# Optimization experiments

Measured on AMD Instinct MI355X. Metric: run time of the kernel, lower is better.

## Reference

```python
import jax, jax.numpy as jnp
import numpy as np

NUM_EMBEDDINGS = 1024
EMBEDDING_DIM = 64
COMMITMENT_COST = 0.25
DECAY = 0.99
EPS = 1e-5


def setup_inputs() -> dict:
    key = jax.random.key(0)
    k1, k2 = jax.random.split(key)
    inputs = jax.random.normal(k1, (32, EMBEDDING_DIM, 64, 64), dtype=jnp.float32)
    scale = 1.0 / NUM_EMBEDDINGS
    embeddings = jax.random.uniform(k2, (NUM_EMBEDDINGS, EMBEDDING_DIM),
                                    dtype=jnp.float32, minval=-scale, maxval=scale)
    return {
        "inputs": inputs,
        "embeddings": embeddings,
        "ema_cluster_size": jnp.zeros((NUM_EMBEDDINGS,), dtype=jnp.float32),
        "ema_w": embeddings.copy(),
    }


def reference(inputs, embeddings, ema_cluster_size, ema_w):
    sg = jax.lax.stop_gradient
    B, C, H, W = inputs.shape          # C == embedding_dim
    K, D = embeddings.shape

    # [B,C,H,W] -> [N,D]
    flat = jnp.transpose(inputs, (0, 2, 3, 1)).reshape(-1, D)

    distances = (jnp.sum(flat * flat, axis=1, keepdims=True)
                 + jnp.sum(embeddings * embeddings, axis=1)
                 - 2.0 * flat @ embeddings.T)
    encoding_indices = jnp.argmin(distances, axis=1)  # [N]

    quantized = embeddings[encoding_indices].reshape(B, H, W, C)
    quantized = jnp.transpose(quantized, (0, 3, 1, 2))  # [B,C,H,W]

    e_latent_loss = jnp.mean((sg(quantized) - inputs) ** 2)
    q_latent_loss = jnp.mean((quantized - sg(inputs)) ** 2)
    vq_loss = q_latent_loss + COMMITMENT_COST * e_latent_loss

    # --- EMA codebook update (no-grad side effect in original) ---
    flat_ng = sg(flat)
    counts = jax.ops.segment_sum(jnp.ones_like(encoding_indices, dtype=flat.dtype),
                                 encoding_indices, num_segments=K)  # == one_hot.sum(0)
    new_cluster_size = ema_cluster_size * DECAY + (1.0 - DECAY) * counts
    # scatter-add of inputs per code (replaces wasteful N*K*D one-hot broadcast)
    embedded_sum = jax.ops.segment_sum(flat_ng, encoding_indices, num_segments=K)
    new_ema_w = ema_w * DECAY + (1.0 - DECAY) * embedded_sum
    n = jnp.sum(new_cluster_size)
    cluster_size = (new_cluster_size + EPS) / (n + K * EPS) * n
    new_embeddings = new_ema_w / cluster_size[:, None]

    # straight-through estimator
    quantized_st = inputs + sg(quantized - inputs)

    return (quantized_st, vq_loss, encoding_indices.reshape(B, H, W),
            new_cluster_size, new_ema_w, new_embeddings)
```

## Files before the change

### kernel.cpp

```cpp
#include <hip/hip_runtime.h>

#define NUM_K 1024
#define DIM 64
#define HWSZ 4096
#define NPIX 131072

#define OUT_Q    0u
#define OUT_LOSS 8388608u
#define OUT_IDX  8388609u
#define OUT_CS   8519681u
#define OUT_EMAW 8520705u
#define OUT_EMB  8586241u

#define WS_SE    0
#define WS_CNT   1024
#define WS_ESUM  2048
#define WS_LOSS  67584
#define WS_NSUM  67585
#define WS_EBF   67840
#define WS_ZERO_BEG 1024
#define WS_ZERO_LEN 66562

#define PIXB   128
#define MARGIN 1.6e-3f

using bf16x8 = __attribute__((ext_vector_type(8))) short;
using f32x4  = __attribute__((ext_vector_type(4))) float;

__device__ __forceinline__ unsigned short f2bf(float f) {
    unsigned u = __float_as_uint(f);
    u += 0x7FFFu + ((u >> 16) & 1u);
    return (unsigned short)(u >> 16);
}

__device__ __forceinline__ float np_sumsq64(const float* __restrict__ a) {
#pragma clang fp contract(off)
    float r0 = a[0] * a[0], r1 = a[1] * a[1], r2 = a[2] * a[2], r3 = a[3] * a[3];
    float r4 = a[4] * a[4], r5 = a[5] * a[5], r6 = a[6] * a[6], r7 = a[7] * a[7];
    for (int i = 8; i < 64; i += 8) {
        r0 += a[i + 0] * a[i + 0];
        r1 += a[i + 1] * a[i + 1];
        r2 += a[i + 2] * a[i + 2];
        r3 += a[i + 3] * a[i + 3];
        r4 += a[i + 4] * a[i + 4];
        r5 += a[i + 5] * a[i + 5];
        r6 += a[i + 6] * a[i + 6];
        r7 += a[i + 7] * a[i + 7];
    }
    return ((r0 + r1) + (r2 + r3)) + ((r4 + r5) + (r6 + r7));
}

__device__ __forceinline__ float np_sumsq64_s(const float* __restrict__ a, int stride) {
#pragma clang fp contract(off)
    float r[8];
#pragma unroll
    for (int j = 0; j < 8; ++j) { const float v = a[j * stride]; r[j] = v * v; }
#pragma unroll
    for (int i = 8; i < 64; i += 8)
#pragma unroll
        for (int j = 0; j < 8; ++j) { const float v = a[(i + j) * stride]; r[j] += v * v; }
    return ((r[0] + r[1]) + (r[2] + r[3])) + ((r[4] + r[5]) + (r[6] + r[7]));
}

__global__ __launch_bounds__(256) void vq_init(const float* __restrict__ emb,
                                               float* __restrict__ ws) {
    const int t = blockIdx.x * 256 + threadIdx.x;
    if (t < WS_ZERO_LEN) ws[WS_ZERO_BEG + t] = 0.0f;
    if (t < NUM_K) ws[WS_SE + t] = np_sumsq64(emb + t * DIM);
    if (t < 8192) {
        const int ct = t >> 7, h = (t >> 6) & 1, ln = t & 63;
        const int code = ct * 16 + (ln & 15), g = ln >> 4;
        const float* er = emb + code * DIM + h * 32 + g * 8;
        unsigned s[8];
#pragma unroll
        for (int e = 0; e < 8; ++e) s[e] = f2bf(er[e]);
        uint4 v = make_uint4(s[0] | (s[1] << 16), s[2] | (s[3] << 16),
                             s[4] | (s[5] << 16), s[6] | (s[7] << 16));
        ((uint4*)(ws + WS_EBF))[t] = v;
    }
}

__global__ __launch_bounds__(256) void vq_main(const float* __restrict__ in,
                                               const float* __restrict__ emb,
                                               float* __restrict__ out,
                                               float* __restrict__ ws) {
    __shared__ __align__(16) float xF[DIM * 132];
    __shared__ __align__(16) float SeL[NUM_K];
    __shared__ float          redM[4][PIXB];
    __shared__ int            cnt_l[PIXB];
    __shared__ unsigned short cand[PIXB * 12];
    __shared__ int            bk[PIXB];
    __shared__ float          wred[4];

    const int t    = threadIdx.x;
    const int lane = t & 63, w = t >> 6;
    const int g    = lane >> 4, cpix = lane & 15;
    const int bid  = blockIdx.x;
    const int b    = bid >> 5;
    const int hw0  = (bid & 31) << 7;
    const int n0   = bid << 7;

    const float* inb = in + (size_t)b * (DIM * HWSZ);

    {
        const float4* s4 = (const float4*)(inb + hw0);
#pragma unroll
        for (int i = 0; i < 8; ++i) {
            const int fi = t + i * 256;
            const int d = fi >> 5, p4 = fi & 31;
            *(float4*)&xF[d * 132 + p4 * 4] = s4[(size_t)d * 1024 + p4];
        }
        ((float4*)SeL)[t] = ((const float4*)(ws + WS_SE))[t];
        if (t < PIXB) cnt_l[t] = 0;
    }
    __syncthreads();

    bf16x8 Bfr[8][2];
#pragma unroll
    for (int tt = 0; tt < 8; ++tt) {
        const int p = tt * 16 + cpix;
#pragma unroll
        for (int h = 0; h < 2; ++h) {
            bf16x8 v;
#pragma unroll
            for (int e = 0; e < 8; ++e)
                v[e] = (short)f2bf(xF[(h * 32 + g * 8 + e) * 132 + p]);
            Bfr[tt][h] = v;
        }
    }
    float Sx = 0.0f;
    if (t < PIXB) Sx = np_sumsq64_s(xF + t, 132);

    const bf16x8* Ef  = (const bf16x8*)(ws + WS_EBF);
    const int     ct0 = w << 4;

    float mn[8];
#pragma unroll
    for (int tt = 0; tt < 8; ++tt) mn[tt] = 3.4e38f;

#pragma unroll 4
    for (int ci = 0; ci < 16; ++ci) {
        const int ct = ct0 + ci;
        const bf16x8 A0 = Ef[(ct * 2 + 0) * 64 + lane];
        const bf16x8 A1 = Ef[(ct * 2 + 1) * 64 + lane];
        const f32x4  se = *(const f32x4*)&SeL[(ct << 4) + (g << 2)];
#pragma unroll
        for (int tt = 0; tt < 8; ++tt) {
            f32x4 acc = {0.f, 0.f, 0.f, 0.f};
            acc = __builtin_amdgcn_mfma_f32_16x16x32_bf16(A0, Bfr[tt][0], acc, 0, 0, 0);
            acc = __builtin_amdgcn_mfma_f32_16x16x32_bf16(A1, Bfr[tt][1], acc, 0, 0, 0);
            const float s0 = fmaf(-2.0f, acc[0], se[0]);
            const float s1 = fmaf(-2.0f, acc[1], se[1]);
            const float s2 = fmaf(-2.0f, acc[2], se[2]);
            const float s3 = fmaf(-2.0f, acc[3], se[3]);
            mn[tt] = fminf(mn[tt], fminf(fminf(s0, s1), fminf(s2, s3)));
        }
    }

#pragma unroll
    for (int tt = 0; tt < 8; ++tt) {
        float m2 = mn[tt];
        m2 = fminf(m2, __shfl_xor(m2, 16, 64));
        m2 = fminf(m2, __shfl_xor(m2, 32, 64));
        if (g == 0) redM[w][tt * 16 + cpix] = m2;
    }
    __syncthreads();
    float thr[8];
#pragma unroll
    for (int tt = 0; tt < 8; ++tt) {
        const int p = tt * 16 + cpix;
        thr[tt] = fminf(fminf(redM[0][p], redM[1][p]),
                        fminf(redM[2][p], redM[3][p])) + MARGIN;
    }

#pragma unroll 4
    for (int ci = 0; ci < 16; ++ci) {
        const int ct = ct0 + ci;
        const bf16x8 A0 = Ef[(ct * 2 + 0) * 64 + lane];
        const bf16x8 A1 = Ef[(ct * 2 + 1) * 64 + lane];
        const f32x4  se = *(const f32x4*)&SeL[(ct << 4) + (g << 2)];
#pragma unroll
        for (int tt = 0; tt < 8; ++tt) {
            f32x4 acc = {0.f, 0.f, 0.f, 0.f};
            acc = __builtin_amdgcn_mfma_f32_16x16x32_bf16(A0, Bfr[tt][0], acc, 0, 0, 0);
            acc = __builtin_amdgcn_mfma_f32_16x16x32_bf16(A1, Bfr[tt][1], acc, 0, 0, 0);
#pragma unroll
            for (int r = 0; r < 4; ++r) {
                const float s = fmaf(-2.0f, acc[r], se[r]);
                if (s <= thr[tt]) {
                    const int p    = tt * 16 + cpix;
                    const int code = (ct << 4) + (g << 2) + r;
                    const int sl   = atomicAdd(&cnt_l[p], 1);
                    if (sl < 12) cand[p * 12 + sl] = (unsigned short)code;
                }
            }
        }
    }
    __syncthreads();

    if (t < PIXB) {
        const int c  = t;
        const int cc = min(cnt_l[c], 12);
        float bd = 3.4e38f; int bi = NUM_K;
        for (int j = 0; j < cc; ++j) {
            const int cd = cand[c * 12 + j];
            const float4* er = (const float4*)(emb + cd * DIM);
            float dot = 0.0f;
#pragma unroll
            for (int i = 0; i < 16; ++i) {
                const float4 e4 = er[i];
                dot = fmaf(xF[(4 * i + 0) * 132 + c], e4.x, dot);
                dot = fmaf(xF[(4 * i + 1) * 132 + c], e4.y, dot);
                dot = fmaf(xF[(4 * i + 2) * 132 + c], e4.z, dot);
                dot = fmaf(xF[(4 * i + 3) * 132 + c], e4.w, dot);
            }
            const float Sec = SeL[cd];
            float dk;
            {
#pragma clang fp contract(off)
                const float tt2 = Sx + Sec;
                dk = tt2 - 2.0f * dot;
            }
            if (dk < bd || (dk == bd && cd < bi)) { bd = dk; bi = cd; }
        }
        bk[c] = bi;
        out[OUT_IDX + n0 + c] = (float)bi;
        atomicAdd(ws + WS_CNT + bi, 1.0f);
    }
    __syncthreads();

    float lsum = 0.0f;
    {
        const int px = t & 127, dh = t >> 7;
        const int id = bk[px];
        float* qp = out + OUT_Q + (size_t)b * (DIM * HWSZ) + hw0 + px;
        const float4* eb4 = (const float4*)(emb + (id << 6) + (dh << 5));
#pragma unroll
        for (int i = 0; i < 8; ++i) {
            const float4 e4 = eb4[i];
            const float ev[4] = {e4.x, e4.y, e4.z, e4.w};
#pragma unroll
            for (int q = 0; q < 4; ++q) {
                const int d = (dh << 5) + i * 4 + q;
                qp[(size_t)d * HWSZ] = ev[q];
                const float df = ev[q] - xF[d * 132 + px];
                lsum = fmaf(df, df, lsum);
            }
        }
    }
#pragma unroll
    for (int off = 32; off > 0; off >>= 1) lsum += __shfl_down(lsum, off, 64);
    if (lane == 0) wred[w] = lsum;
    __syncthreads();
    if (t == 0) atomicAdd(ws + WS_LOSS, (wred[0] + wred[1]) + (wred[2] + wred[3]));

    {
        float* es = ws + WS_ESUM;
#pragma unroll 1
        for (int j = 0; j < 32; ++j) {
            const int p   = (w << 5) + j;
            const int pid = bk[p];
            atomicAdd(es + (pid << 6) + lane, xF[lane * 132 + p]);
        }
    }
}

__global__ __launch_bounds__(256) void vq_cs(const float* __restrict__ ema_cs,
                                             float* __restrict__ out,
                                             float* __restrict__ ws) {
    const int k = blockIdx.x * 256 + threadIdx.x;
    const float ncs = fmaf(0.01f, ws[WS_CNT + k], 0.99f * ema_cs[k]);
    out[OUT_CS + k] = ncs;
    float s = ncs;
#pragma unroll
    for (int off = 32; off > 0; off >>= 1) s += __shfl_down(s, off, 64);
    if ((threadIdx.x & 63) == 0) atomicAdd(ws + WS_NSUM, s);
}

__global__ __launch_bounds__(256) void vq_final_b(const float* __restrict__ ema_w,
                                                  float* __restrict__ out,
                                                  float* __restrict__ ws) {
    const int i = blockIdx.x * 256 + threadIdx.x;
    const int k = i >> 6;
    const float nsum = ws[WS_NSUM];
    const float ncs  = out[OUT_CS + k];
    const float csz  = (ncs + 1e-5f) / (nsum + 1024.0f * 1e-5f) * nsum;
    const float nw   = fmaf(0.01f, ws[WS_ESUM + i], 0.99f * ema_w[i]);
    out[OUT_EMAW + i] = nw;
    out[OUT_EMB  + i] = nw / csz;
    if (i == 0) out[OUT_LOSS] = 1.25f * ws[WS_LOSS] * (1.0f / 8388608.0f);
}

extern "C" void kernel_launch(void* const* d_in, const int* in_sizes, int n_in,
                              void* d_out, int out_size, void* d_ws, size_t ws_size,
                              hipStream_t stream) {
    const float* in   = (const float*)d_in[0];
    const float* emb  = (const float*)d_in[1];
    const float* ecs  = (const float*)d_in[2];
    const float* emaw = (const float*)d_in[3];
    float* out = (float*)d_out;
    float* ws  = (float*)d_ws;

    vq_init<<<261, 256, 0, stream>>>(emb, ws);
    vq_main<<<NPIX / PIXB, 256, 0, stream>>>(in, emb, out, ws);
    vq_cs<<<4, 256, 0, stream>>>(ecs, out, ws);
    vq_final_b<<<256, 256, 0, stream>>>(emaw, out, ws);
}
```

Before: 216.0 us.

## Halve pixels per block, pad smem stride, fuse cluster-size kernel into final

Cuts the per-block pixel tile from 128 to 64, which doubles the grid to 2048 blocks and halves per-thread B fragments and LDS use. It sets launch bounds to request 5 waves-per-EU-level occupancy and changes the xF stride to 65 to avoid bank conflicts. It also folds the cluster-size kernel into the final kernel: each block redundantly recomputes the total count sum, which removes one launch and one global atomic. In exchange, every codebook fragment is reloaded from global for only half as many pixels, and the scalar LDS stores replace float4 stores.

```diff
diff --git a/kernel.cpp b/kernel.cpp
--- a/kernel.cpp
+++ b/kernel.cpp
@@ -16,12 +16,12 @@
 #define WS_CNT   1024
 #define WS_ESUM  2048
 #define WS_LOSS  67584
-#define WS_NSUM  67585
 #define WS_EBF   67840
 #define WS_ZERO_BEG 1024
-#define WS_ZERO_LEN 66562
-
-#define PIXB   128
+#define WS_ZERO_LEN 66561
+
+#define PIXB   64
+#define XSTR   65
 #define MARGIN 1.6e-3f
 
 using bf16x8 = __attribute__((ext_vector_type(8))) short;
@@ -80,13 +80,13 @@
     }
 }
 
-__global__ __launch_bounds__(256) void vq_main(const float* __restrict__ in,
-                                               const float* __restrict__ emb,
-                                               float* __restrict__ out,
-                                               float* __restrict__ ws) {
-    __shared__ __align__(16) float xF[DIM * 132];
-    __shared__ __align__(16) float SeL[NUM_K];
-    __shared__ float          redM[4][PIXB];
+__global__ __launch_bounds__(256, 5) void vq_main(const float* __restrict__ in,
+                                                  const float* __restrict__ emb,
+                                                  float* __restrict__ out,
+                                                  float* __restrict__ ws) {
+    __shared__ float xF[DIM * XSTR];
+    __shared__ float SeL[NUM_K];
+    __shared__ float redM[4][PIXB];
     __shared__ int            cnt_l[PIXB];
     __shared__ unsigned short cand[PIXB * 12];
     __shared__ int            bk[PIXB];
@@ -96,47 +96,49 @@
     const int lane = t & 63, w = t >> 6;
     const int g    = lane >> 4, cpix = lane & 15;
     const int bid  = blockIdx.x;
-    const int b    = bid >> 5;
-    const int hw0  = (bid & 31) << 7;
-    const int n0   = bid << 7;
+    const int b    = bid >> 6;
+    const int hw0  = (bid & 63) << 6;
+    const int n0   = bid << 6;
 
     const float* inb = in + (size_t)b * (DIM * HWSZ);
 
     {
         const float4* s4 = (const float4*)(inb + hw0);
 #pragma unroll
-        for (int i = 0; i < 8; ++i) {
+        for (int i = 0; i < 4; ++i) {
             const int fi = t + i * 256;
-            const int d = fi >> 5, p4 = fi & 31;
-            *(float4*)&xF[d * 132 + p4 * 4] = s4[(size_t)d * 1024 + p4];
+            const int d = fi >> 4, p4 = fi & 15;
+            const float4 v = s4[(size_t)d * 1024 + p4];
+            float* dst = &xF[d * XSTR + p4 * 4];
+            dst[0] = v.x; dst[1] = v.y; dst[2] = v.z; dst[3] = v.w;
         }
         ((float4*)SeL)[t] = ((const float4*)(ws + WS_SE))[t];
         if (t < PIXB) cnt_l[t] = 0;
     }
     __syncthreads();
 
-    bf16x8 Bfr[8][2];
-#pragma unroll
-    for (int tt = 0; tt < 8; ++tt) {
+    bf16x8 Bfr[4][2];
+#pragma unroll
+    for (int tt = 0; tt < 4; ++tt) {
         const int p = tt * 16 + cpix;
 #pragma unroll
         for (int h = 0; h < 2; ++h) {
             bf16x8 v;
 #pragma unroll
             for (int e = 0; e < 8; ++e)
-                v[e] = (short)f2bf(xF[(h * 32 + g * 8 + e) * 132 + p]);
+                v[e] = (short)f2bf(xF[(h * 32 + g * 8 + e) * XSTR + p]);
             Bfr[tt][h] = v;
         }
     }
     float Sx = 0.0f;
-    if (t < PIXB) Sx = np_sumsq64_s(xF + t, 132);
+    if (t < PIXB) Sx = np_sumsq64_s(xF + t, XSTR);
 
     const bf16x8* Ef  = (const bf16x8*)(ws + WS_EBF);
     const int     ct0 = w << 4;
 
-    float mn[8];
-#pragma unroll
-    for (int tt = 0; tt < 8; ++tt) mn[tt] = 3.4e38f;
+    float mn[4];
+#pragma unroll
+    for (int tt = 0; tt < 4; ++tt) mn[tt] = 3.4e38f;
 
 #pragma unroll 4
     for (int ci = 0; ci < 16; ++ci) {
@@ -145,7 +147,7 @@
         const bf16x8 A1 = Ef[(ct * 2 + 1) * 64 + lane];
         const f32x4  se = *(const f32x4*)&SeL[(ct << 4) + (g << 2)];
 #pragma unroll
-        for (int tt = 0; tt < 8; ++tt) {
+        for (int tt = 0; tt < 4; ++tt) {
             f32x4 acc = {0.f, 0.f, 0.f, 0.f};
             acc = __builtin_amdgcn_mfma_f32_16x16x32_bf16(A0, Bfr[tt][0], acc, 0, 0, 0);
             acc = __builtin_amdgcn_mfma_f32_16x16x32_bf16(A1, Bfr[tt][1], acc, 0, 0, 0);
@@ -153,21 +155,21 @@
             const float s1 = fmaf(-2.0f, acc[1], se[1]);
             const float s2 = fmaf(-2.0f, acc[2], se[2]);
             const float s3 = fmaf(-2.0f, acc[3], se[3]);
-            mn[tt] = fminf(mn[tt], fminf(fminf(s0, s1), fminf(s2, s3)));
-        }
-    }
-
-#pragma unroll
-    for (int tt = 0; tt < 8; ++tt) {
+            mn[tt] = fminf(fminf(fminf(s0, s1), fminf(s2, s3)), mn[tt]);
+        }
+    }
+
+#pragma unroll
+    for (int tt = 0; tt < 4; ++tt) {
         float m2 = mn[tt];
         m2 = fminf(m2, __shfl_xor(m2, 16, 64));
         m2 = fminf(m2, __shfl_xor(m2, 32, 64));
         if (g == 0) redM[w][tt * 16 + cpix] = m2;
     }
     __syncthreads();
-    float thr[8];
-#pragma unroll
-    for (int tt = 0; tt < 8; ++tt) {
+    float thr[4];
+#pragma unroll
+    for (int tt = 0; tt < 4; ++tt) {
         const int p = tt * 16 + cpix;
         thr[tt] = fminf(fminf(redM[0][p], redM[1][p]),
                         fminf(redM[2][p], redM[3][p])) + MARGIN;
@@ -178,12 +180,12 @@
         const int ct = ct0 + ci;
         const bf16x8 A0 = Ef[(ct * 2 + 0) * 64 + lane];
         const bf16x8 A1 = Ef[(ct * 2 + 1) * 64 + lane];
-        const f32x4  se = *(const f32x4*)&SeL[(ct << 4) + (g << 2)];
-#pragma unroll
-        for (int tt = 0; tt < 8; ++tt) {
+#pragma unroll
+        for (int tt = 0; tt < 4; ++tt) {
             f32x4 acc = {0.f, 0.f, 0.f, 0.f};
             acc = __builtin_amdgcn_mfma_f32_16x16x32_bf16(A0, Bfr[tt][0], acc, 0, 0, 0);
             acc = __builtin_amdgcn_mfma_f32_16x16x32_bf16(A1, Bfr[tt][1], acc, 0, 0, 0);
+            const f32x4 se = *(const f32x4*)&SeL[(ct << 4) + (g << 2)];
 #pragma unroll
             for (int r = 0; r < 4; ++r) {
                 const float s = fmaf(-2.0f, acc[r], se[r]);
@@ -209,10 +211,10 @@
 #pragma unroll
             for (int i = 0; i < 16; ++i) {
                 const float4 e4 = er[i];
-                dot = fmaf(xF[(4 * i + 0) * 132 + c], e4.x, dot);
-                dot = fmaf(xF[(4 * i + 1) * 132 + c], e4.y, dot);
-                dot = fmaf(xF[(4 * i + 2) * 132 + c], e4.z, dot);
-                dot = fmaf(xF[(4 * i + 3) * 132 + c], e4.w, dot);
+                dot = fmaf(xF[(4 * i + 0) * XSTR + c], e4.x, dot);
+                dot = fmaf(xF[(4 * i + 1) * XSTR + c], e4.y, dot);
+                dot = fmaf(xF[(4 * i + 2) * XSTR + c], e4.z, dot);
+                dot = fmaf(xF[(4 * i + 3) * XSTR + c], e4.w, dot);
             }
             const float Sec = SeL[cd];
             float dk;
@@ -231,19 +233,19 @@
 
     float lsum = 0.0f;
     {
-        const int px = t & 127, dh = t >> 7;
+        const int px = t & 63, dq = t >> 6;
         const int id = bk[px];
         float* qp = out + OUT_Q + (size_t)b * (DIM * HWSZ) + hw0 + px;
-        const float4* eb4 = (const float4*)(emb + (id << 6) + (dh << 5));
-#pragma unroll
-        for (int i = 0; i < 8; ++i) {
+        const float4* eb4 = (const float4*)(emb + (id << 6) + (dq << 4));
+#pragma unroll
+        for (int i = 0; i < 4; ++i) {
             const float4 e4 = eb4[i];
             const float ev[4] = {e4.x, e4.y, e4.z, e4.w};
 #pragma unroll
             for (int q = 0; q < 4; ++q) {
-                const int d = (dh << 5) + i * 4 + q;
+                const int d = (dq << 4) + i * 4 + q;
                 qp[(size_t)d * HWSZ] = ev[q];
-                const float df = ev[q] - xF[d * 132 + px];
+                const float df = ev[q] - xF[d * XSTR + px];
                 lsum = fmaf(df, df, lsum);
             }
         }
@@ -257,35 +259,46 @@
     {
         float* es = ws + WS_ESUM;
 #pragma unroll 1
-        for (int j = 0; j < 32; ++j) {
-            const int p   = (w << 5) + j;
+        for (int j = 0; j < 16; ++j) {
+            const int p   = (w << 4) + j;
             const int pid = bk[p];
-            atomicAdd(es + (pid << 6) + lane, xF[lane * 132 + p]);
-        }
-    }
-}
-
-__global__ __launch_bounds__(256) void vq_cs(const float* __restrict__ ema_cs,
-                                             float* __restrict__ out,
-                                             float* __restrict__ ws) {
-    const int k = blockIdx.x * 256 + threadIdx.x;
+            atomicAdd(es + (pid << 6) + lane, xF[lane * XSTR + p]);
+        }
+    }
+}
+
+__global__ __launch_bounds__(256) void vq_final(const float* __restrict__ ema_cs,
+                                                const float* __restrict__ ema_w,
+                                                float* __restrict__ out,
+                                                float* __restrict__ ws) {
+    __shared__ float nred[4];
+    const int t = threadIdx.x, lane = t & 63, w = t >> 6;
+
+    float s = 0.0f;
+#pragma unroll
+    for (int j = 0; j < 4; ++j) {
+        const int k = t + j * 256;
+        s += fmaf(0.01f, ws[WS_CNT + k], 0.99f * ema_cs[k]);
+    }
+#pragma unroll
+    for (int off = 32; off > 0; off >>= 1) s += __shfl_down(s, off, 64);
+    if (lane == 0) nred[w] = s;
+    __syncthreads();
+    const float nsum = (nred[0] + nred[1]) + (nred[2] + nred[3]);
+
+    if (blockIdx.x == 0) {
+#pragma unroll
+        for (int j = 0; j < 4; ++j) {
+            const int k = t + j * 256;
+            out[OUT_CS + k] = fmaf(0.01f, ws[WS_CNT + k], 0.99f * ema_cs[k]);
+        }
+    }
+
+    const int i = blockIdx.x * 256 + t;
+    const int k = i >> 6;
     const float ncs = fmaf(0.01f, ws[WS_CNT + k], 0.99f * ema_cs[k]);
-    out[OUT_CS + k] = ncs;
-    float s = ncs;
-#pragma unroll
-    for (int off = 32; off > 0; off >>= 1) s += __shfl_down(s, off, 64);
-    if ((threadIdx.x & 63) == 0) atomicAdd(ws + WS_NSUM, s);
-}
-
-__global__ __launch_bounds__(256) void vq_final_b(const float* __restrict__ ema_w,
-                                                  float* __restrict__ out,
-                                                  float* __restrict__ ws) {
-    const int i = blockIdx.x * 256 + threadIdx.x;
-    const int k = i >> 6;
-    const float nsum = ws[WS_NSUM];
-    const float ncs  = out[OUT_CS + k];
-    const float csz  = (ncs + 1e-5f) / (nsum + 1024.0f * 1e-5f) * nsum;
-    const float nw   = fmaf(0.01f, ws[WS_ESUM + i], 0.99f * ema_w[i]);
+    const float csz = (ncs + 1e-5f) / (nsum + 1024.0f * 1e-5f) * nsum;
+    const float nw  = fmaf(0.01f, ws[WS_ESUM + i], 0.99f * ema_w[i]);
     out[OUT_EMAW + i] = nw;
     out[OUT_EMB  + i] = nw / csz;
     if (i == 0) out[OUT_LOSS] = 1.25f * ws[WS_LOSS] * (1.0f / 8388608.0f);
@@ -303,6 +316,5 @@
 
     vq_init<<<261, 256, 0, stream>>>(emb, ws);
     vq_main<<<NPIX / PIXB, 256, 0, stream>>>(in, emb, out, ws);
-    vq_cs<<<4, 256, 0, stream>>>(ecs, out, ws);
-    vq_final_b<<<256, 256, 0, stream>>>(emaw, out, ws);
-}
+    vq_final<<<256, 256, 0, stream>>>(ecs, emaw, out, ws);
+}
```

Result: faster. 201.9 us (-6.6%).
